# Performance work log

Hardware: AMD Instinct MI355X
Metric: run time of the kernel (lower is better)

The kernel has to match this reference:

```python
import jax, jax.numpy as jnp
import numpy as np
from jax import lax

DIM = 512
HEADS = 8
HID = 128           # FRN hidden_dim
DIM_CONV = DIM // 4 # 128, partial-conv channels
EPS = 1e-5


def layernorm(x, g, b):
    mu = jnp.mean(x, axis=-1, keepdims=True)
    var = jnp.mean((x - mu) ** 2, axis=-1, keepdims=True)
    return (x - mu) * lax.rsqrt(var + EPS) * g + b


def conv2d(x, w, groups=1):
    # x: (N,C,H,W), w: (O, C/groups, kh, kw), stride 1, SAME padding
    return lax.conv_general_dilated(x, w, (1, 1), 'SAME',
                                    dimension_numbers=('NCHW', 'OIHW', 'NCHW'),
                                    feature_group_count=groups)


def setup_inputs() -> dict:
    key = jax.random.key(0)
    ks = jax.random.split(key, 12)
    s = 0.02
    inp = {
        'x': jax.random.normal(ks[0], (196, 256, DIM), dtype=jnp.float32),
        'ln1_g': jnp.ones((DIM,), jnp.float32),
        'ln1_b': jnp.zeros((DIM,), jnp.float32),
        'qkv_w': jax.random.normal(ks[1], (DIM, 3 * DIM), jnp.float32) * s,
        'proj_w': jax.random.normal(ks[2], (DIM, DIM), jnp.float32) * s,
        'proj_b': jnp.zeros((DIM,), jnp.float32),
        'ln2_g': jnp.ones((DIM,), jnp.float32),
        'ln2_b': jnp.zeros((DIM,), jnp.float32),
        'pconv_w': jax.random.normal(ks[3], (DIM_CONV, DIM_CONV, 3, 3), jnp.float32) * s,
        'lin1_w': jax.random.normal(ks[4], (DIM, 2 * HID), jnp.float32) * s,
        'lin1_b': jnp.zeros((2 * HID,), jnp.float32),
        'dw_w': jax.random.normal(ks[5], (HID, 1, 3, 3), jnp.float32) * s,
        'dw_b': jnp.zeros((HID,), jnp.float32),
        'lin2_w': jax.random.normal(ks[6], (HID, DIM), jnp.float32) * s,
        'lin2_b': jnp.zeros((DIM,), jnp.float32),
    }
    return inp


def reference(x, ln1_g, ln1_b, qkv_w, proj_w, proj_b, ln2_g, ln2_b,
              pconv_w, lin1_w, lin1_b, dw_w, dw_b, lin2_w, lin2_b):
    B, N, C = x.shape
    hd = C // HEADS
    scale = hd ** -0.5

    # ---- SQAttention on norm1(x) ----
    h = layernorm(x, ln1_g, ln1_b)
    qkv = (h @ qkv_w).reshape(B, N, 3, HEADS, hd)
    q, k, v = qkv[:, :, 0], qkv[:, :, 1], qkv[:, :, 2]  # (B,N,H,hd)
    attn = jnp.einsum('bnhd,bmhd->bhnm', q, k) * scale   # (B,H,N,N)
    # sigmoid mask from the LAST query row, averaged over heads
    mask = jax.nn.sigmoid(jnp.mean(attn[:, :, -1, :], axis=1))[:, None, None, :]  # (B,1,1,N)
    attn = jax.nn.softmax(attn, axis=-1) * mask
    o = jnp.einsum('bhnm,bmhd->bnhd', attn, v).reshape(B, N, C)
    x = x + (o @ proj_w + proj_b)

    # ---- FRN on norm2(x): treats axis0 as (h w)=hw, axis1 as batch ----
    y = layernorm(x, ln2_g, ln2_b)
    hw, bs, c = y.shape
    hh = int(np.sqrt(hw))
    yi = y.reshape(hh, hh, bs, c).transpose(2, 3, 0, 1)  # (bs,c,hh,hh)
    y1 = conv2d(yi[:, :DIM_CONV], pconv_w)               # partial conv, no bias
    yi = jnp.concatenate([y1, yi[:, DIM_CONV:]], axis=1)
    y = yi.transpose(2, 3, 0, 1).reshape(hw, bs, c)      # (hw,bs,c)
    y = jax.nn.gelu(y @ lin1_w + lin1_b, approximate=False)
    y_1, y_2 = y[..., :HID], y[..., HID:]
    y1i = y_1.reshape(hh, hh, bs, HID).transpose(2, 3, 0, 1)
    y1i = jax.nn.gelu(conv2d(y1i, dw_w, groups=HID) + dw_b[None, :, None, None],
                      approximate=False)
    y_1 = y1i.transpose(2, 3, 0, 1).reshape(hw, bs, HID)
    y = (y_1 * y_2) @ lin2_w + lin2_b
    return x + y
```

## Files before the change

kernel.cpp:

```cpp
#include <hip/hip_runtime.h>
#include <hip/hip_bf16.h>

#define NB   196
#define NT   256
#define CDIM 512
#define NH   8
#define MROWS 50176
#define HB   98
#define MH   (HB*NT)

typedef __attribute__((ext_vector_type(8))) short short8;
typedef __attribute__((ext_vector_type(4))) float f32x4;
typedef __attribute__((ext_vector_type(4))) unsigned uint32x4;

__device__ __forceinline__ float gelu_f(float x) {
    return 0.5f * x * (1.0f + erff(x * 0.70710678118654752440f));
}
__device__ __forceinline__ float b2f(unsigned u) { return __uint_as_float(u << 16); }
__device__ __forceinline__ unsigned f2b(float f) {
    __hip_bfloat16 h = __float2bfloat16(f);
    return (unsigned)__builtin_bit_cast(unsigned short, h);
}
__device__ __forceinline__ unsigned pk2(float a, float b) { return f2b(a) | (f2b(b) << 16); }
__device__ __forceinline__ void u4_to_f8(uint4 v, float* f) {
    f[0] = b2f(v.x & 0xffffu); f[1] = b2f(v.x >> 16);
    f[2] = b2f(v.y & 0xffffu); f[3] = b2f(v.y >> 16);
    f[4] = b2f(v.z & 0xffffu); f[5] = b2f(v.z >> 16);
    f[6] = b2f(v.w & 0xffffu); f[7] = b2f(v.w >> 16);
}
__device__ __forceinline__ void gload_lds16(const void* g, void* l) {
    __builtin_amdgcn_global_load_lds(
        (const __attribute__((address_space(1))) void*)g,
        (__attribute__((address_space(3))) void*)l, 16, 0, 0);
}

__global__ __launch_bounds__(256) void convert_wT_kernel(
    const float* __restrict__ w, unsigned short* __restrict__ wT, int K, int N)
{
    int o = blockIdx.x * 256 + threadIdx.x;
    if (o >= K * N) return;
    int k = o / N, n = o - k * N;
    wT[(size_t)n * K + k] = (unsigned short)f2b(w[o]);
}
__global__ __launch_bounds__(256) void convert_kernel(
    const float* __restrict__ w, unsigned short* __restrict__ wT, int n)
{
    int o = blockIdx.x * 256 + threadIdx.x;
    if (o < n) wT[o] = (unsigned short)f2b(w[o]);
}

template<int INBF>
__global__ __launch_bounds__(64) void ln_kernel(
    const void* __restrict__ inp, const float* __restrict__ g,
    const float* __restrict__ b, unsigned short* __restrict__ out)
{
    int row = blockIdx.x;
    int lane = threadIdx.x;
    float f[8];
    if constexpr (INBF) {
        const unsigned short* p = (const unsigned short*)inp + (size_t)row * CDIM + lane * 8;
        uint4 v = *(const uint4*)p;
        u4_to_f8(v, f);
    } else {
        const float* p = (const float*)inp + (size_t)row * CDIM + lane * 8;
        float4 a = *(const float4*)p;
        float4 c = *(const float4*)(p + 4);
        f[0]=a.x; f[1]=a.y; f[2]=a.z; f[3]=a.w; f[4]=c.x; f[5]=c.y; f[6]=c.z; f[7]=c.w;
    }
    float s = 0;
#pragma unroll
    for (int i = 0; i < 8; ++i) s += f[i];
#pragma unroll
    for (int off = 1; off < 64; off <<= 1) s += __shfl_xor(s, off);
    float mu = s * (1.0f / 512.0f);
    float sq = 0;
#pragma unroll
    for (int i = 0; i < 8; ++i) { f[i] -= mu; sq += f[i] * f[i]; }
#pragma unroll
    for (int off = 1; off < 64; off <<= 1) sq += __shfl_xor(sq, off);
    float inv = rsqrtf(sq * (1.0f / 512.0f) + 1e-5f);
    float4 g0 = *(const float4*)(g + lane * 8);
    float4 g1 = *(const float4*)(g + lane * 8 + 4);
    float4 b0 = *(const float4*)(b + lane * 8);
    float4 b1 = *(const float4*)(b + lane * 8 + 4);
    float r0 = f[0]*inv*g0.x + b0.x, r1 = f[1]*inv*g0.y + b0.y;
    float r2 = f[2]*inv*g0.z + b0.z, r3 = f[3]*inv*g0.w + b0.w;
    float r4 = f[4]*inv*g1.x + b1.x, r5 = f[5]*inv*g1.y + b1.y;
    float r6 = f[6]*inv*g1.z + b1.z, r7 = f[7]*inv*g1.w + b1.w;
    uint4 ov = { pk2(r0, r1), pk2(r2, r3), pk2(r4, r5), pk2(r6, r7) };
    *(uint4*)(out + (size_t)row * CDIM + lane * 8) = ov;
}

template<typename TC, int RES, int CONV>
__global__ __launch_bounds__(256) void gemm_mfma(
    const unsigned short* __restrict__ A,
    const unsigned short* __restrict__ BT,
    const float* __restrict__ bias,
    const void* __restrict__ resid,
    TC* __restrict__ C,
    int K, int lda, int ldc, int act, int NBM, int NBN)
{
    __shared__ __align__(16) unsigned short As[3][128][32];
    __shared__ __align__(16) unsigned short Bs[3][128][32];
    int lin = blockIdx.x;
    int xcd = lin & 7;
    int rr = lin >> 3;
    int nb = rr % NBN;
    int pb = rr / NBN;
    int mb = (pb << 3) + xcd;
    if (mb >= NBM) return;
    int m0 = mb << 7;
    int n0 = nb << 7;

    int tid = threadIdx.x;
    int lane = tid & 63;
    int wave = tid >> 6;
    int wr = wave >> 1, wc = wave & 1;
    int fr = lane & 15;
    int fg = lane >> 4;

    int rsub = lane >> 2;
    int cch = lane & 3;
    int csrc = (cch ^ (rsub & 3)) << 3;

    int i0 = 0, j0 = 0, bs0 = 0;
    if constexpr (CONV) {
        int hw = m0 >> 8;
        i0 = hw / 14; j0 = hw - i0 * 14;
        bs0 = m0 & 255;
    }

    auto stage = [&](int bf, int k0) {
        if constexpr (CONV) {
            int kl = tid & 31;
            int mq = (tid >> 5) << 4;
            int k = k0 + kl;
            int ci = k / 9; int r9 = k - ci * 9;
            int di = r9 / 3; int dj = r9 - di * 3;
            int ii = i0 + di - 1, jj = j0 + dj - 1;
            uint4 v0 = {0,0,0,0}, v1 = {0,0,0,0};
            if ((unsigned)ii < 14u && (unsigned)jj < 14u) {
                const unsigned short* src = A + (size_t)ci * MROWS + (size_t)(ii * 14 + jj) * 256 + bs0 + mq;
                v0 = *(const uint4*)src;
                v1 = *(const uint4*)(src + 8);
            }
            unsigned short e[16];
            *(uint4*)&e[0] = v0; *(uint4*)&e[8] = v1;
            int ch = kl >> 3, wi = kl & 7;
#pragma unroll
            for (int e2 = 0; e2 < 16; ++e2)
                As[bf][mq + e2][((ch ^ (e2 & 3)) << 3) + wi] = e[e2];
        } else {
#pragma unroll
            for (int t = 0; t < 2; ++t) {
                int seg = (wave << 1) + t;
                int row = (seg << 4) + rsub;
                gload_lds16(A + (size_t)(m0 + row) * lda + k0 + csrc,
                            (char*)&As[bf][0][0] + (seg << 10));
            }
        }
#pragma unroll
        for (int t = 0; t < 2; ++t) {
            int seg = (wave << 1) + t;
            int row = (seg << 4) + rsub;
            gload_lds16(BT + (size_t)(n0 + row) * K + k0 + csrc,
                        (char*)&Bs[bf][0][0] + (seg << 10));
        }
    };

    f32x4 acc[4][4];
#pragma unroll
    for (int i = 0; i < 4; ++i)
#pragma unroll
        for (int j = 0; j < 4; ++j) acc[i][j] = (f32x4){0.f, 0.f, 0.f, 0.f};

    int nsteps = K >> 5;
    stage(0, 0);
    if (nsteps > 1) {
        stage(1, 32);
        asm volatile("s_waitcnt vmcnt(4)" ::: "memory");
    } else {
        asm volatile("s_waitcnt vmcnt(0)" ::: "memory");
    }
    __builtin_amdgcn_s_barrier();

    for (int s = 0; s < nsteps; ++s) {
        int bcur = s % 3;
        if (s + 2 < nsteps) stage((s + 2) % 3, (s + 2) << 5);
        int chl = (fg ^ (fr & 3)) << 3;
        short8 af[4], bfr[4];
#pragma unroll
        for (int i = 0; i < 4; ++i)
            af[i] = *(const short8*)&As[bcur][(wr << 6) + (i << 4) + fr][chl];
#pragma unroll
        for (int j = 0; j < 4; ++j)
            bfr[j] = *(const short8*)&Bs[bcur][(wc << 6) + (j << 4) + fr][chl];
#pragma unroll
        for (int i = 0; i < 4; ++i)
#pragma unroll
            for (int j = 0; j < 4; ++j)
                acc[i][j] = __builtin_amdgcn_mfma_f32_16x16x32_bf16(af[i], bfr[j], acc[i][j], 0, 0, 0);
        if (s + 1 < nsteps) {
            if (s + 2 < nsteps) asm volatile("s_waitcnt vmcnt(4) lgkmcnt(0)" ::: "memory");
            else                asm volatile("s_waitcnt vmcnt(0) lgkmcnt(0)" ::: "memory");
            __builtin_amdgcn_s_barrier();
        }
    }

#pragma unroll
    for (int i = 0; i < 4; ++i) {
        int rowb = m0 + (wr << 6) + (i << 4) + ((lane >> 4) << 2);
#pragma unroll
        for (int j = 0; j < 4; ++j) {
            int col = n0 + (wc << 6) + (j << 4) + fr;
            float bj = bias ? bias[col] : 0.0f;
#pragma unroll
            for (int r = 0; r < 4; ++r) {
                int row = rowb + r;
                float v = acc[i][j][r] + bj;
                if constexpr (RES == 1)
                    v += ((const float*)resid)[(size_t)row * ldc + col];
                else if constexpr (RES == 2)
                    v += b2f(((const unsigned short*)resid)[(size_t)row * ldc + col]);
                if (act) v = gelu_f(v);
                if constexpr (sizeof(TC) == 4)
                    ((float*)C)[(size_t)row * ldc + col] = v;
                else
                    ((unsigned short*)C)[(size_t)row * ldc + col] = (unsigned short)f2b(v);
            }
        }
    }
}
static inline int xcd_grid(int NBM, int NBN) { return 8 * ((NBM + 7) / 8) * NBN; }

__global__ __launch_bounds__(256) void mask_kernel(
    const unsigned short* __restrict__ qkv, float* __restrict__ mk)
{
    __shared__ float ql[512];
    int b = blockIdx.x, tid = threadIdx.x;
    const unsigned short* qlast = qkv + ((size_t)(b * NT + 255) * 3) * CDIM;
    ql[tid] = b2f(qlast[tid]);
    ql[tid + 256] = b2f(qlast[tid + 256]);
    __syncthreads();
    const unsigned short* kp = qkv + ((size_t)(b * NT + tid) * 3 + 1) * CDIM;
    float s = 0;
    for (int cq = 0; cq < 512; cq += 8) {
        uint4 kv = *(const uint4*)(kp + cq);
        float f[8];
        u4_to_f8(kv, f);
#pragma unroll
        for (int q = 0; q < 8; ++q) s += ql[cq + q] * f[q];
    }
    s *= 0.015625f;
    mk[b * NT + tid] = 1.0f / (1.0f + __expf(-s));
}

__global__ __launch_bounds__(512) void attn_mfma(
    const unsigned short* __restrict__ qkv, const float* __restrict__ mask,
    unsigned short* __restrict__ o)
{
    __shared__ __align__(16) unsigned short smem[128][64];
    int h = blockIdx.x, b = blockIdx.y;
    int tid = threadIdx.x;
    int lane = tid & 63;
    int wid = tid >> 6;
    int fr = lane & 15;
    int fg = lane >> 4;
    const unsigned short* base = qkv + (size_t)b * NT * 3 * CDIM + h * 64;

    short8 qf[2][2];
#pragma unroll
    for (int t = 0; t < 2; ++t)
#pragma unroll
        for (int kc = 0; kc < 2; ++kc)
            qf[t][kc] = *(const short8*)(base +
                (size_t)((wid << 5) + (t << 4) + fr) * 3 * CDIM + (kc << 5) + (fg << 3));

    f32x4 oacc[2][4];
#pragma unroll
    for (int t = 0; t < 2; ++t)
#pragma unroll
        for (int n = 0; n < 4; ++n) oacc[t][n] = (f32x4){0.f, 0.f, 0.f, 0.f};
    float l[2] = {0.f, 0.f};

    int srcA = ((fg & 1) << 5) + fr;

    for (int c = 0; c < 4; ++c) {
        __syncthreads();
        {
            int kr = tid >> 3, ch = tid & 7;
            int gm = (c << 6) + kr;
            uint4 kv = *(const uint4*)(base + (size_t)(gm * 3 + 1) * CDIM + (ch << 3));
            *(uint4*)&smem[kr][(ch ^ (kr & 7)) << 3] = kv;
            float mv = mask[b * NT + gm];
            uint4 vv = *(const uint4*)(base + (size_t)(gm * 3 + 2) * CDIM + (ch << 3));
            float f[8];
            u4_to_f8(vv, f);
#pragma unroll
            for (int e = 0; e < 8; ++e) {
                int d = (ch << 3) + e;
                smem[64 + d][(((kr >> 3) ^ (d & 7)) << 3) + (kr & 7)] = (unsigned short)f2b(f[e] * mv);
            }
        }
        __syncthreads();
        short8 kf[4][2];
#pragma unroll
        for (int j = 0; j < 4; ++j)
#pragma unroll
            for (int kc = 0; kc < 2; ++kc)
                kf[j][kc] = *(const short8*)&smem[(j << 4) + fr][((((kc << 2) + fg) ^ (fr & 7)) << 3)];
        short8 vf[4][2];
#pragma unroll
        for (int n = 0; n < 4; ++n)
#pragma unroll
            for (int kc2 = 0; kc2 < 2; ++kc2)
                vf[n][kc2] = *(const short8*)&smem[64 + (n << 4) + fr][((((kc2 << 2) + fg) ^ (fr & 7)) << 3)];
#pragma unroll
        for (int t = 0; t < 2; ++t) {
            f32x4 sa[4];
#pragma unroll
            for (int j = 0; j < 4; ++j) sa[j] = (f32x4){0.f, 0.f, 0.f, 0.f};
#pragma unroll
            for (int kc = 0; kc < 2; ++kc)
#pragma unroll
                for (int j = 0; j < 4; ++j)
                    sa[j] = __builtin_amdgcn_mfma_f32_16x16x32_bf16(kf[j][kc], qf[t][kc], sa[j], 0, 0, 0);
            float p[4][4];
            float ls = 0.f;
#pragma unroll
            for (int j = 0; j < 4; ++j)
#pragma unroll
                for (int r = 0; r < 4; ++r) {
                    p[j][r] = __expf(sa[j][r] * 0.125f);
                    ls += p[j][r];
                }
            ls += __shfl_xor(ls, 16);
            ls += __shfl_xor(ls, 32);
            l[t] += ls;
            unsigned pkv[4][2];
#pragma unroll
            for (int j = 0; j < 4; ++j) {
                pkv[j][0] = pk2(p[j][0], p[j][1]);
                pkv[j][1] = pk2(p[j][2], p[j][3]);
            }
#pragma unroll
            for (int kc2 = 0; kc2 < 2; ++kc2) {
                unsigned w0[4], w1[4];
                w0[0] = __shfl(pkv[(kc2 << 1) + 0][0], srcA);
                w0[1] = __shfl(pkv[(kc2 << 1) + 0][1], srcA);
                w0[2] = __shfl(pkv[(kc2 << 1) + 0][0], srcA + 16);
                w0[3] = __shfl(pkv[(kc2 << 1) + 0][1], srcA + 16);
                w1[0] = __shfl(pkv[(kc2 << 1) + 1][0], srcA);
                w1[1] = __shfl(pkv[(kc2 << 1) + 1][1], srcA);
                w1[2] = __shfl(pkv[(kc2 << 1) + 1][0], srcA + 16);
                w1[3] = __shfl(pkv[(kc2 << 1) + 1][1], srcA + 16);
                bool hi = fg >= 2;
                uint32x4 pw = { hi ? w1[0] : w0[0], hi ? w1[1] : w0[1],
                                hi ? w1[2] : w0[2], hi ? w1[3] : w0[3] };
                short8 pf = __builtin_bit_cast(short8, pw);
#pragma unroll
                for (int n = 0; n < 4; ++n)
                    oacc[t][n] = __builtin_amdgcn_mfma_f32_16x16x32_bf16(pf, vf[n][kc2], oacc[t][n], 0, 0, 0);
            }
        }
    }

#pragma unroll
    for (int half = 0; half < 2; ++half) {
        __syncthreads();
        if ((wid >> 2) == half) {
            int qr = (wid & 3) << 5;
#pragma unroll
            for (int t = 0; t < 2; ++t) {
                float invl = 1.0f / l[t];
                float rl[4];
#pragma unroll
                for (int r = 0; r < 4; ++r)
                    rl[r] = __shfl(invl, (fg << 2) + r);
#pragma unroll
                for (int n = 0; n < 4; ++n)
#pragma unroll
                    for (int r = 0; r < 4; ++r) {
                        int row = qr + (t << 4) + (fg << 2) + r;
                        int d = (n << 4) + fr;
                        smem[row][((((d >> 3) ^ (row & 7)) << 3)) | (d & 7)] =
                            (unsigned short)f2b(oacc[t][n][r] * rl[r]);
                    }
            }
        }
        __syncthreads();
#pragma unroll
        for (int p = 0; p < 2; ++p) {
            int idx = tid + (p << 9);
            int row = idx >> 3;
            int ch = idx & 7;
            uint4 ov = *(const uint4*)&smem[row][(ch ^ (row & 7)) << 3];
            *(uint4*)(o + (size_t)(b * NT + (half << 7) + row) * CDIM + h * 64 + (ch << 3)) = ov;
        }
    }
}

__global__ __launch_bounds__(256) void transpose_kernel(
    const unsigned short* __restrict__ y, unsigned short* __restrict__ yT)
{
    int g = blockIdx.x * 256 + threadIdx.x;
    int row = g >> 4;
    int cq = (g & 15) << 3;
    uint4 v = *(const uint4*)(y + (size_t)row * CDIM + cq);
    unsigned short e[8] = {
        (unsigned short)(v.x & 0xffffu), (unsigned short)(v.x >> 16),
        (unsigned short)(v.y & 0xffffu), (unsigned short)(v.y >> 16),
        (unsigned short)(v.z & 0xffffu), (unsigned short)(v.z >> 16),
        (unsigned short)(v.w & 0xffffu), (unsigned short)(v.w >> 16) };
    int hw = row >> 8, bs = row & 255;
    size_t off = (size_t)cq * MROWS + (size_t)hw * 256 + bs;
#pragma unroll
    for (int i = 0; i < 8; ++i) yT[off + (size_t)i * MROWS] = e[i];
}

__global__ __launch_bounds__(256) void dwconv_kernel(
    const unsigned short* __restrict__ u, const float* __restrict__ w,
    const float* __restrict__ wb, unsigned short* __restrict__ y1)
{
    int hw = blockIdx.x;
    int i = hw / 14;
    int j = hw - i * 14;
    int tid = threadIdx.x;
    int c = (tid & 31) << 2;
    int bs = (blockIdx.y << 3) + (tid >> 5);
    float a0 = 0, a1 = 0, a2 = 0, a3 = 0;
#pragma unroll
    for (int di = 0; di < 3; ++di) {
        int ii = i + di - 1;
        if ((unsigned)ii >= 14u) continue;
#pragma unroll
        for (int dj = 0; dj < 3; ++dj) {
            int jj = j + dj - 1;
            if ((unsigned)jj >= 14u) continue;
            int r = di * 3 + dj;
            uint2 uv = *(const uint2*)(u + ((size_t)(ii * 14 + jj) * 256 + bs) * 256 + c);
            a0 += w[(c + 0) * 9 + r] * b2f(uv.x & 0xffffu);
            a1 += w[(c + 1) * 9 + r] * b2f(uv.x >> 16);
            a2 += w[(c + 2) * 9 + r] * b2f(uv.y & 0xffffu);
            a3 += w[(c + 3) * 9 + r] * b2f(uv.y >> 16);
        }
    }
    a0 = gelu_f(a0 + wb[c]);
    a1 = gelu_f(a1 + wb[c + 1]);
    a2 = gelu_f(a2 + wb[c + 2]);
    a3 = gelu_f(a3 + wb[c + 3]);
    uint2 g2 = *(const uint2*)(u + ((size_t)hw * 256 + bs) * 256 + 128 + c);
    a0 *= b2f(g2.x & 0xffffu); a1 *= b2f(g2.x >> 16);
    a2 *= b2f(g2.y & 0xffffu); a3 *= b2f(g2.y >> 16);
    ushort4 ov = { (unsigned short)f2b(a0), (unsigned short)f2b(a1),
                   (unsigned short)f2b(a2), (unsigned short)f2b(a3) };
    *(ushort4*)(y1 + ((size_t)hw * 256 + bs) * 128 + c) = ov;
}

extern "C" void kernel_launch(void* const* d_in, const int* in_sizes, int n_in,
                              void* d_out, int out_size, void* d_ws, size_t ws_size,
                              hipStream_t stream)
{
    (void)in_sizes; (void)n_in; (void)out_size; (void)ws_size;
    const float* x      = (const float*)d_in[0];
    const float* ln1_g  = (const float*)d_in[1];
    const float* ln1_b  = (const float*)d_in[2];
    const float* qkv_w  = (const float*)d_in[3];
    const float* proj_w = (const float*)d_in[4];
    const float* proj_b = (const float*)d_in[5];
    const float* ln2_g  = (const float*)d_in[6];
    const float* ln2_b  = (const float*)d_in[7];
    const float* pconv_w= (const float*)d_in[8];
    const float* lin1_w = (const float*)d_in[9];
    const float* lin1_b = (const float*)d_in[10];
    const float* dw_w   = (const float*)d_in[11];
    const float* dw_b   = (const float*)d_in[12];
    const float* lin2_w = (const float*)d_in[13];
    const float* lin2_b = (const float*)d_in[14];
    float* out = (float*)d_out;

    unsigned short* Ob   = (unsigned short*)d_out;
    unsigned short* o_bf = Ob;
    unsigned short* h_bf = Ob + 25690112;
    float* mk            = (float*)(Ob + 25690112 + 12845056);
    unsigned short* y_bf = Ob;
    unsigned short* yT_b = Ob + 25690112;

    unsigned short* ws16   = (unsigned short*)d_ws;
    unsigned short* qkvW   = ws16;
    unsigned short* projW  = ws16 + 786432;
    unsigned short* pconvW = ws16 + 1048576;
    unsigned short* lin1W  = ws16 + 1196032;
    unsigned short* lin2W  = ws16 + 1327104;
    unsigned short* qkv_b  = ws16 + 1392640;
    unsigned short* x2_b   = ws16 + 1392640;
    unsigned short* u_b    = ws16 + 27082752;
    unsigned short* y1_b   = ws16 + 39927808;

    convert_wT_kernel<<<3072, 256, 0, stream>>>(qkv_w,  qkvW,  512, 1536);
    convert_wT_kernel<<<1024, 256, 0, stream>>>(proj_w, projW, 512, 512);
    convert_kernel  <<< 576, 256, 0, stream>>>(pconv_w, pconvW, 147456);
    convert_wT_kernel<<< 512, 256, 0, stream>>>(lin1_w, lin1W, 512, 256);
    convert_wT_kernel<<< 256, 256, 0, stream>>>(lin2_w, lin2W, 128, 512);

    for (int r = 0; r < 2; ++r) {
        const float* xr = x + (size_t)r * MH * CDIM;
        ln_kernel<0><<<MH, 64, 0, stream>>>(xr, ln1_g, ln1_b, h_bf);
        gemm_mfma<unsigned short, 0, 0><<<xcd_grid(196, 12), 256, 0, stream>>>(
            h_bf, qkvW, nullptr, nullptr, qkv_b, 512, 512, 1536, 0, 196, 12);
        mask_kernel<<<HB, 256, 0, stream>>>(qkv_b, mk + (size_t)r * HB * NT);
        attn_mfma<<<dim3(NH, HB), 512, 0, stream>>>(
            qkv_b, mk + (size_t)r * HB * NT, o_bf + (size_t)r * MH * CDIM);
    }
    gemm_mfma<unsigned short, 1, 0><<<xcd_grid(392, 4), 256, 0, stream>>>(
        o_bf, projW, proj_b, x, x2_b, 512, 512, 512, 0, 392, 4);
    ln_kernel<1><<<MROWS, 64, 0, stream>>>(x2_b, ln2_g, ln2_b, y_bf);
    transpose_kernel<<<3136, 256, 0, stream>>>(y_bf, yT_b);
    gemm_mfma<unsigned short, 0, 1><<<xcd_grid(392, 1), 256, 0, stream>>>(
        yT_b, pconvW, nullptr, nullptr, y_bf, 1152, 0, 512, 0, 392, 1);
    gemm_mfma<unsigned short, 0, 0><<<xcd_grid(392, 2), 256, 0, stream>>>(
        y_bf, lin1W, lin1_b, nullptr, u_b, 512, 512, 256, 1, 392, 2);
    dwconv_kernel<<<dim3(NB, 32), 256, 0, stream>>>(u_b, dw_w, dw_b, y1_b);
    gemm_mfma<float, 2, 0><<<xcd_grid(392, 4), 256, 0, stream>>>(
        y1_b, lin2W, lin2_b, x2_b, out, 128, 128, 512, 0, 392, 4);
}
```

Baseline: 745.1 us.

## Add 256x256-tile 8-wave MFMA GEMM with 16x16x32 bf16 and use for dense GEMMs

Introduces a new GEMM kernel with 256x256 output tiles, 512 threads (8 waves, 2x4 arrangement), K-step 64 double-buffered via direct global-to-LDS loads with XOR swizzle, and 16x16x32 bf16 MFMA in quadrant order with setprio hints. The qkv, proj, lin1 and lin2 GEMMs switch to it, meaning more data reuse per block and fewer blocks. The trade-offs are larger register and LDS use, fewer blocks to fill the CUs (lin1 gets only 196 blocks), and an epilogue that still writes scalar elements.

```diff
diff --git a/kernel.cpp b/kernel.cpp
--- a/kernel.cpp
+++ b/kernel.cpp
@@ -33,6 +33,7 @@
         (const __attribute__((address_space(1))) void*)g,
         (__attribute__((address_space(3))) void*)l, 16, 0, 0);
 }
+static inline int xcd_grid(int NBM, int NBN) { return 8 * ((NBM + 7) / 8) * NBN; }
 
 __global__ __launch_bounds__(256) void convert_wT_kernel(
     const float* __restrict__ w, unsigned short* __restrict__ wT, int K, int N)
@@ -89,6 +90,147 @@
     float r6 = f[6]*inv*g1.z + b1.z, r7 = f[7]*inv*g1.w + b1.w;
     uint4 ov = { pk2(r0, r1), pk2(r2, r3), pk2(r4, r5), pk2(r6, r7) };
     *(uint4*)(out + (size_t)row * CDIM + lane * 8) = ov;
+}
+
+#define QUAD16(MH, NH) \
+    __builtin_amdgcn_s_setprio(1); \
+    _Pragma("unroll") \
+    for (int mi2 = 0; mi2 < 4; ++mi2) \
+        _Pragma("unroll") \
+        for (int nj2 = 0; nj2 < 2; ++nj2) \
+            _Pragma("unroll") \
+            for (int kk = 0; kk < 2; ++kk) \
+                acc[(MH)*4 + mi2][(NH)*2 + nj2] = __builtin_amdgcn_mfma_f32_16x16x32_bf16( \
+                    afr[mi2][kk], bfr[nj2][kk], acc[(MH)*4 + mi2][(NH)*2 + nj2], 0, 0, 0); \
+    __builtin_amdgcn_s_setprio(0);
+
+template<typename TC, int RES>
+__global__ __launch_bounds__(512, 2) void gemm_mfma256(
+    const unsigned short* __restrict__ A,
+    const unsigned short* __restrict__ BT,
+    const float* __restrict__ bias,
+    const void* __restrict__ resid,
+    TC* __restrict__ C,
+    int K, int lda, int ldc, int act, int NBM, int NBN)
+{
+    __shared__ __align__(16) unsigned short As[2][256][64];
+    __shared__ __align__(16) unsigned short Bs[2][256][64];
+    int lin = blockIdx.x;
+    int xcd = lin & 7;
+    int rr = lin >> 3;
+    int nb = rr % NBN;
+    int pb = rr / NBN;
+    int mb = (pb << 3) + xcd;
+    if (mb >= NBM) return;
+    int m0 = mb << 8;
+    int n0 = nb << 8;
+
+    int tid = threadIdx.x;
+    int lane = tid & 63;
+    int wave = tid >> 6;
+    int wr = wave >> 2;
+    int wc = wave & 3;
+    int fr = lane & 15;
+    int fg = lane >> 4;
+
+    int rsub8 = lane >> 3;
+    int cch = lane & 7;
+
+    auto stage = [&](int p, int k0) {
+#pragma unroll
+        for (int tI = 0; tI < 4; ++tI) {
+            int seg = (wave << 2) + tI;
+            int row = (seg << 3) + rsub8;
+            int csrc = (cch ^ (row & 7)) << 3;
+            gload_lds16(A + (size_t)(m0 + row) * lda + k0 + csrc,
+                        (char*)&As[p][0][0] + (seg << 10));
+        }
+#pragma unroll
+        for (int tI = 0; tI < 4; ++tI) {
+            int seg = (wave << 2) + tI;
+            int row = (seg << 3) + rsub8;
+            int csrc = (cch ^ (row & 7)) << 3;
+            gload_lds16(BT + (size_t)(n0 + row) * K + k0 + csrc,
+                        (char*)&Bs[p][0][0] + (seg << 10));
+        }
+    };
+
+    f32x4 acc[8][4];
+#pragma unroll
+    for (int i = 0; i < 8; ++i)
+#pragma unroll
+        for (int j = 0; j < 4; ++j) acc[i][j] = (f32x4){0.f, 0.f, 0.f, 0.f};
+
+    short8 afr[4][2];
+    short8 bfr[2][2];
+
+    auto loadA = [&](int p, int mh) {
+#pragma unroll
+        for (int mi2 = 0; mi2 < 4; ++mi2)
+#pragma unroll
+            for (int kk = 0; kk < 2; ++kk) {
+                int row = (wr << 7) + (mh << 6) + (mi2 << 4) + fr;
+                int ch = ((kk << 2) + fg) ^ (row & 7);
+                afr[mi2][kk] = *(const short8*)&As[p][row][ch << 3];
+            }
+    };
+    auto loadB = [&](int p, int nh) {
+#pragma unroll
+        for (int nj2 = 0; nj2 < 2; ++nj2)
+#pragma unroll
+            for (int kk = 0; kk < 2; ++kk) {
+                int row = (wc << 6) + (nh << 5) + (nj2 << 4) + fr;
+                int ch = ((kk << 2) + fg) ^ (row & 7);
+                bfr[nj2][kk] = *(const short8*)&Bs[p][row][ch << 3];
+            }
+    };
+
+    int NKT = K >> 6;
+    stage(0, 0);
+    asm volatile("s_waitcnt vmcnt(0)" ::: "memory");
+    __builtin_amdgcn_s_barrier();
+
+    for (int t = 0; t < NKT; ++t) {
+        int p = t & 1;
+        if (t + 1 < NKT) stage(p ^ 1, (t + 1) << 6);
+        loadA(p, 0); loadB(p, 0);
+        QUAD16(0, 0)
+        __builtin_amdgcn_s_barrier();
+        loadB(p, 1);
+        QUAD16(0, 1)
+        __builtin_amdgcn_s_barrier();
+        loadA(p, 1);
+        QUAD16(1, 1)
+        __builtin_amdgcn_s_barrier();
+        loadB(p, 0);
+        QUAD16(1, 0)
+        if (t + 1 < NKT) asm volatile("s_waitcnt vmcnt(0)" ::: "memory");
+        __builtin_amdgcn_s_barrier();
+    }
+
+#pragma unroll
+    for (int mi = 0; mi < 8; ++mi) {
+        int rowb = m0 + (wr << 7) + (mi << 4) + (fg << 2);
+#pragma unroll
+        for (int nj = 0; nj < 4; ++nj) {
+            int col = n0 + (wc << 6) + (nj << 4) + fr;
+            float bj = bias ? bias[col] : 0.0f;
+#pragma unroll
+            for (int r = 0; r < 4; ++r) {
+                int row = rowb + r;
+                float v = acc[mi][nj][r] + bj;
+                if constexpr (RES == 1)
+                    v += ((const float*)resid)[(size_t)row * ldc + col];
+                else if constexpr (RES == 2)
+                    v += b2f(((const unsigned short*)resid)[(size_t)row * ldc + col]);
+                if (act) v = gelu_f(v);
+                if constexpr (sizeof(TC) == 4)
+                    ((float*)C)[(size_t)row * ldc + col] = v;
+                else
+                    ((unsigned short*)C)[(size_t)row * ldc + col] = (unsigned short)f2b(v);
+            }
+        }
+    }
 }
 
 template<typename TC, int RES, int CONV>
@@ -231,7 +373,6 @@
         }
     }
 }
-static inline int xcd_grid(int NBM, int NBN) { return 8 * ((NBM + 7) / 8) * NBN; }
 
 __global__ __launch_bounds__(256) void mask_kernel(
     const unsigned short* __restrict__ qkv, float* __restrict__ mk)
@@ -506,21 +647,21 @@
     for (int r = 0; r < 2; ++r) {
         const float* xr = x + (size_t)r * MH * CDIM;
         ln_kernel<0><<<MH, 64, 0, stream>>>(xr, ln1_g, ln1_b, h_bf);
-        gemm_mfma<unsigned short, 0, 0><<<xcd_grid(196, 12), 256, 0, stream>>>(
-            h_bf, qkvW, nullptr, nullptr, qkv_b, 512, 512, 1536, 0, 196, 12);
+        gemm_mfma256<unsigned short, 0><<<xcd_grid(98, 6), 512, 0, stream>>>(
+            h_bf, qkvW, nullptr, nullptr, qkv_b, 512, 512, 1536, 0, 98, 6);
         mask_kernel<<<HB, 256, 0, stream>>>(qkv_b, mk + (size_t)r * HB * NT);
         attn_mfma<<<dim3(NH, HB), 512, 0, stream>>>(
             qkv_b, mk + (size_t)r * HB * NT, o_bf + (size_t)r * MH * CDIM);
     }
-    gemm_mfma<unsigned short, 1, 0><<<xcd_grid(392, 4), 256, 0, stream>>>(
-        o_bf, projW, proj_b, x, x2_b, 512, 512, 512, 0, 392, 4);
+    gemm_mfma256<unsigned short, 1><<<xcd_grid(196, 2), 512, 0, stream>>>(
+        o_bf, projW, proj_b, x, x2_b, 512, 512, 512, 0, 196, 2);
     ln_kernel<1><<<MROWS, 64, 0, stream>>>(x2_b, ln2_g, ln2_b, y_bf);
     transpose_kernel<<<3136, 256, 0, stream>>>(y_bf, yT_b);
     gemm_mfma<unsigned short, 0, 1><<<xcd_grid(392, 1), 256, 0, stream>>>(
         yT_b, pconvW, nullptr, nullptr, y_bf, 1152, 0, 512, 0, 392, 1);
-    gemm_mfma<unsigned short, 0, 0><<<xcd_grid(392, 2), 256, 0, stream>>>(
-        y_bf, lin1W, lin1_b, nullptr, u_b, 512, 512, 256, 1, 392, 2);
+    gemm_mfma256<unsigned short, 0><<<xcd_grid(196, 1), 512, 0, stream>>>(
+        y_bf, lin1W, lin1_b, nullptr, u_b, 512, 512, 256, 1, 196, 1);
     dwconv_kernel<<<dim3(NB, 32), 256, 0, stream>>>(u_b, dw_w, dw_b, y1_b);
-    gemm_mfma<float, 2, 0><<<xcd_grid(392, 4), 256, 0, stream>>>(
-        y1_b, lin2W, lin2_b, x2_b, out, 128, 128, 512, 0, 392, 4);
-}
+    gemm_mfma256<float, 2><<<xcd_grid(196, 2), 512, 0, stream>>>(
+        y1_b, lin2W, lin2_b, x2_b, out, 128, 128, 512, 0, 196, 2);
+}
```

After: 855.1 us. 1.15x slower.
